# Optimization experiments

Measured on AMD Instinct MI355X. Metric: run time of the kernel, lower is better.

The kernel has to match this reference:

```python
import jax, jax.numpy as jnp
import numpy as np

B, S, D = 4, 2048, 1024
EPS = 1e-5


def setup_inputs() -> dict:
    key = jax.random.key(0)
    ks = jax.random.split(key, 8)
    s = 1.0 / np.sqrt(D)
    return {
        "x": jax.random.normal(ks[0], (B, S, D), dtype=jnp.float32),
        "Wq": jax.random.normal(ks[1], (D, D), dtype=jnp.float32) * s,
        "Wk": jax.random.normal(ks[2], (D, D), dtype=jnp.float32) * s,
        "Wv": jax.random.normal(ks[3], (D, D), dtype=jnp.float32) * s,
        "W1": jax.random.normal(ks[4], (D, D), dtype=jnp.float32) * s,
        "b1": jnp.zeros((D,), dtype=jnp.float32),
        "W2": jax.random.normal(ks[5], (D, D), dtype=jnp.float32) * s,
        "b2": jnp.zeros((D,), dtype=jnp.float32),
        "gamma": jnp.ones((D,), dtype=jnp.float32),
        "beta": jnp.zeros((D,), dtype=jnp.float32),
    }


def _layer_norm(x, gamma, beta):
    mu = jnp.mean(x, axis=-1, keepdims=True)
    var = jnp.mean(jnp.square(x - mu), axis=-1, keepdims=True)
    return (x - mu) * jax.lax.rsqrt(var + EPS) * gamma + beta


def reference(x, Wq, Wk, Wv, W1, b1, W2, b2, gamma, beta):
    seq_len, d = x.shape[1], x.shape[2]
    # torch Linear: y = x @ W.T
    Q = jnp.einsum('bsd,ed->bse', x, Wq)
    K = jnp.einsum('bsd,ed->bse', x, Wk)
    V = jnp.einsum('bsd,ed,->bse', x, Wv, jnp.float32(1.0)) if False else jnp.einsum('bsd,ed->bse', x, Wv)
    scores = jnp.einsum('bqd,bkd->bqk', Q, K) / jnp.sqrt(jnp.float32(d))
    causal = jnp.tril(jnp.ones((seq_len, seq_len), dtype=bool))  # [S,S]
    scores = jnp.where(causal[None, :, :], scores, -jnp.inf)
    attn = jax.nn.softmax(scores, axis=-1)
    attn_out = jnp.einsum('bqk,bkd->bqd', attn, V)
    # dropout is identity at eval
    h = _layer_norm(x + attn_out, gamma, beta)
    ff = jnp.einsum('bsd,ed->bse', jax.nn.relu(jnp.einsum('bsd,ed->bse', h, W1) + b1), W2) + b2
    out = _layer_norm(h + ff, gamma, beta)
    return out
```

## Files before the change

### kernel.cpp

```cpp
#include <hip/hip_runtime.h>
#include <math.h>
#include <cstdint>
#include <cstddef>

#define DI __device__ __forceinline__

typedef __bf16 bf16x8 __attribute__((ext_vector_type(8)));
typedef float f32x4 __attribute__((ext_vector_type(4)));

static constexpr int kB = 4, kS = 2048, kD = 1024;
static constexpr int kM = kB * kS;
static constexpr float kScale = 0.03125f;
static constexpr float kEps = 1e-5f;

DI unsigned short f2bf(float f) {
  unsigned u = __float_as_uint(f);
  u += 0x7FFFu + ((u >> 16) & 1u);
  return (unsigned short)(u >> 16);
}

DI void gld_lds16(const void* g, void* l) {
  __builtin_amdgcn_global_load_lds(
      (__attribute__((address_space(1))) void*)(void*)g,
      (__attribute__((address_space(3))) void*)l, 16, 0, 0);
}

__global__ __launch_bounds__(256) void k_cast_all(
    const float* __restrict__ x, const float* __restrict__ Wq,
    const float* __restrict__ Wk, const float* __restrict__ Wv,
    const float* __restrict__ W1, const float* __restrict__ W2,
    unsigned short* __restrict__ xb, unsigned short* __restrict__ Wqkvb,
    unsigned short* __restrict__ W1b, unsigned short* __restrict__ W2b) {
  const int i = blockIdx.x * 256 + threadIdx.x;
  const int X4 = kM * kD / 4;
  const int W4 = kD * kD / 4;
  const float* src;
  unsigned short* dst;
  int j;
  if (i < X4) { src = x; dst = xb; j = i; }
  else if (i < X4 + W4)     { src = Wq; dst = Wqkvb;           j = i - X4; }
  else if (i < X4 + 2 * W4) { src = Wk; dst = Wqkvb + 4 * W4;  j = i - X4 - W4; }
  else if (i < X4 + 3 * W4) { src = Wv; dst = Wqkvb + 8 * W4;  j = i - X4 - 2 * W4; }
  else if (i < X4 + 4 * W4) { src = W1; dst = W1b;             j = i - X4 - 3 * W4; }
  else                      { src = W2; dst = W2b;             j = i - X4 - 4 * W4; }
  float4 v = ((const float4*)src)[j];
  ushort4 o;
  o.x = f2bf(v.x); o.y = f2bf(v.y); o.z = f2bf(v.z); o.w = f2bf(v.w);
  ((ushort4*)dst)[j] = o;
}

template <int OUT_BF16, int RELU, int CAUSAL>
__global__ __launch_bounds__(256, 2) void k_gemm_nt(
    const unsigned short* __restrict__ A, const unsigned short* __restrict__ B,
    void* __restrict__ Cv, const float* __restrict__ bias,
    int M, int N, int K, int lda, int ldb, int ldc,
    long sA, long sB, long sC) {
  int bm, bn;
  if (CAUSAL == 1) {
    const int t = blockIdx.x;
    int r = (int)floorf((sqrtf(8.f * (float)t + 1.f) - 1.f) * 0.5f);
    while ((r + 1) * (r + 2) / 2 <= t) ++r;
    while (r * (r + 1) / 2 > t) --r;
    bm = r * 128;
    bn = (t - r * (r + 1) / 2) * 128;
  } else if (CAUSAL == 2) {
    bm = (gridDim.y - 1 - blockIdx.y) * 128;
    bn = blockIdx.x * 128;
  } else {
    bm = blockIdx.y * 128;
    bn = blockIdx.x * 128;
  }
  A += (long)blockIdx.z * sA;
  B += (long)blockIdx.z * sB;
  const int Keff = (CAUSAL == 2) ? ((K < bm + 128) ? K : bm + 128) : K;

  const int tid = threadIdx.x;
  const int lane = tid & 63;
  const int wm = ((tid >> 6) >> 1) * 64;
  const int wn = ((tid >> 6) & 1) * 64;

  __shared__ __align__(16) unsigned short Asm[128 * 64];
  __shared__ __align__(16) unsigned short Bsm[128 * 64];

  f32x4 acc[4][4];
#pragma unroll
  for (int i = 0; i < 4; ++i)
#pragma unroll
    for (int j = 0; j < 4; ++j) acc[i][j] = (f32x4){0.f, 0.f, 0.f, 0.f};

  const int r_row = tid >> 3;
  const int dst_k = (tid & 7) * 8;
  const int src_k = ((tid & 7) ^ ((tid >> 3) & 7)) * 8;
  const int fm = lane & 15;
  const int fq = lane >> 4;

  for (int k0 = 0; k0 < Keff; k0 += 64) {
#pragma unroll
    for (int i = 0; i < 4; ++i) {
      const int row = i * 32 + r_row;
      gld_lds16(A + (long)(bm + row) * lda + (k0 + src_k), Asm + row * 64 + dst_k);
      gld_lds16(B + (long)(bn + row) * ldb + (k0 + src_k), Bsm + row * 64 + dst_k);
    }
    __syncthreads();
#pragma unroll
    for (int kk = 0; kk < 2; ++kk) {
      bf16x8 af[4], bfr[4];
#pragma unroll
      for (int i = 0; i < 4; ++i) {
        const int pa = ((kk * 4 + fq) ^ (fm & 7)) * 8;
        af[i]  = *(const bf16x8*)(Asm + (wm + i * 16 + fm) * 64 + pa);
        bfr[i] = *(const bf16x8*)(Bsm + (wn + i * 16 + fm) * 64 + pa);
      }
#pragma unroll
      for (int i = 0; i < 4; ++i)
#pragma unroll
        for (int j = 0; j < 4; ++j)
          acc[i][j] = __builtin_amdgcn_mfma_f32_16x16x32_bf16(af[i], bfr[j], acc[i][j], 0, 0, 0);
    }
    __syncthreads();
  }

  const long cb = (long)blockIdx.z * sC;
#pragma unroll
  for (int i = 0; i < 4; ++i) {
#pragma unroll
    for (int j = 0; j < 4; ++j) {
      const int col = bn + wn + j * 16 + fm;
      const float bv = bias ? bias[col] : 0.f;
#pragma unroll
      for (int r = 0; r < 4; ++r) {
        const int row = bm + wm + i * 16 + fq * 4 + r;
        float v = acc[i][j][r] + bv;
        if (RELU) v = fmaxf(v, 0.f);
        if (OUT_BF16)
          ((unsigned short*)Cv)[cb + (long)row * ldc + col] = f2bf(v);
        else
          ((float*)Cv)[cb + (long)row * ldc + col] = v;
      }
    }
  }
}

DI float wsum(float v) {
  v += __shfl_xor(v, 32, 64);
  v += __shfl_xor(v, 16, 64);
  v += __shfl_xor(v, 8, 64);
  v += __shfl_xor(v, 4, 64);
  v += __shfl_xor(v, 2, 64);
  v += __shfl_xor(v, 1, 64);
  return v;
}
DI float wmax(float v) {
  v = fmaxf(v, __shfl_xor(v, 32, 64));
  v = fmaxf(v, __shfl_xor(v, 16, 64));
  v = fmaxf(v, __shfl_xor(v, 8, 64));
  v = fmaxf(v, __shfl_xor(v, 4, 64));
  v = fmaxf(v, __shfl_xor(v, 2, 64));
  v = fmaxf(v, __shfl_xor(v, 1, 64));
  return v;
}

__global__ __launch_bounds__(256) void k_softmax_causal(const float* __restrict__ S,
                                                        unsigned short* __restrict__ P) {
  const int row = blockIdx.x;
  const int q = row & (kS - 1);
  const int lim = (q & ~127) + 128;
  const float* Srow = S + (long)row * kS;
  unsigned short* Prow = P + (long)row * kS;
  const int tid = threadIdx.x;
  __shared__ float red[4];

  float v[8];
  float mx = -INFINITY;
#pragma unroll
  for (int i = 0; i < 8; ++i) {
    const int k = tid + i * 256;
    float xv = -INFINITY;
    if (k <= q) xv = Srow[k] * kScale;
    v[i] = xv;
    mx = fmaxf(mx, xv);
  }
  mx = wmax(mx);
  if ((tid & 63) == 0) red[tid >> 6] = mx;
  __syncthreads();
  mx = fmaxf(fmaxf(red[0], red[1]), fmaxf(red[2], red[3]));
  __syncthreads();

  float sum = 0.f;
#pragma unroll
  for (int i = 0; i < 8; ++i) {
    const float e = (v[i] > -INFINITY) ? __expf(v[i] - mx) : 0.f;
    v[i] = e;
    sum += e;
  }
  sum = wsum(sum);
  if ((tid & 63) == 0) red[tid >> 6] = sum;
  __syncthreads();
  sum = red[0] + red[1] + red[2] + red[3];
  const float inv = 1.f / sum;
#pragma unroll
  for (int i = 0; i < 8; ++i) {
    const int k = tid + i * 256;
    if (k < lim) Prow[k] = f2bf(v[i] * inv);
  }
}

template <int WRITE_BF16>
__global__ __launch_bounds__(256) void k_residual_ln(
    const float* __restrict__ X, const float* __restrict__ Y,
    const float* __restrict__ gamma, const float* __restrict__ beta,
    float* __restrict__ Out, unsigned short* __restrict__ OutB) {
  const long base = (long)blockIdx.x * kD;
  const int tid = threadIdx.x;
  __shared__ float reds[4], redss[4];
  float v[4];
  float s = 0.f, ss2 = 0.f;
#pragma unroll
  for (int i = 0; i < 4; ++i) {
    const int k = tid + i * 256;
    const float xv = X[base + k] + Y[base + k];
    v[i] = xv;
    s += xv;
    ss2 += xv * xv;
  }
  s = wsum(s);
  ss2 = wsum(ss2);
  if ((tid & 63) == 0) { reds[tid >> 6] = s; redss[tid >> 6] = ss2; }
  __syncthreads();
  s = reds[0] + reds[1] + reds[2] + reds[3];
  ss2 = redss[0] + redss[1] + redss[2] + redss[3];
  const float mu = s * (1.f / kD);
  float var = ss2 * (1.f / kD) - mu * mu;
  var = fmaxf(var, 0.f);
  const float rstd = rsqrtf(var + kEps);
#pragma unroll
  for (int i = 0; i < 4; ++i) {
    const int k = tid + i * 256;
    const float y = (v[i] - mu) * rstd * gamma[k] + beta[k];
    Out[base + k] = y;
    if (WRITE_BF16) OutB[base + k] = f2bf(y);
  }
}

__global__ __launch_bounds__(256) void k_transpose_bf16(
    const unsigned short* __restrict__ in, unsigned short* __restrict__ out,
    int rows, int cols, int ld_in, int ld_out, long sIn, long sOut) {
  __shared__ unsigned short tile[64][65];
  const long ib = (long)blockIdx.z * sIn;
  const long ob = (long)blockIdx.z * sOut;
  const int c0 = blockIdx.x * 64, r0 = blockIdx.y * 64;
  const int tx = threadIdx.x & 63;
  const int ty = threadIdx.x >> 6;
#pragma unroll
  for (int i = 0; i < 16; ++i) {
    const int r = ty + i * 4;
    tile[r][tx] = in[ib + (long)(r0 + r) * ld_in + (c0 + tx)];
  }
  __syncthreads();
#pragma unroll
  for (int i = 0; i < 16; ++i) {
    const int c = ty + i * 4;
    out[ob + (long)(c0 + c) * ld_out + (r0 + tx)] = tile[tx][c];
  }
}

extern "C" void kernel_launch(void* const* d_in, const int* in_sizes, int n_in,
                              void* d_out, int out_size, void* d_ws, size_t ws_size,
                              hipStream_t stream) {
  (void)in_sizes; (void)n_in; (void)out_size; (void)ws_size;
  const float* x     = (const float*)d_in[0];
  const float* Wq    = (const float*)d_in[1];
  const float* Wk    = (const float*)d_in[2];
  const float* Wv    = (const float*)d_in[3];
  const float* W1    = (const float*)d_in[4];
  const float* b1    = (const float*)d_in[5];
  const float* W2    = (const float*)d_in[6];
  const float* b2    = (const float*)d_in[7];
  const float* gamma = (const float*)d_in[8];
  const float* beta  = (const float*)d_in[9];
  float* out = (float*)d_out;

  char* base = (char*)d_ws;
  size_t off = 0;
  auto alloc = [&](size_t bytes) -> void* {
    void* p = base + off;
    off = (off + bytes + 255) & ~(size_t)255;
    return p;
  };

  unsigned short* xb    = (unsigned short*)alloc((size_t)kM * kD * 2);
  unsigned short* Wqkvb = (unsigned short*)alloc((size_t)3 * kD * kD * 2);
  unsigned short* W1b   = (unsigned short*)alloc((size_t)kD * kD * 2);
  unsigned short* W2b   = (unsigned short*)alloc((size_t)kD * kD * 2);
  unsigned short* QKVb  = (unsigned short*)alloc((size_t)kM * 3 * kD * 2);
  unsigned short* Vt    = (unsigned short*)alloc((size_t)kM * kD * 2);
  float*          scores = (float*)alloc((size_t)kB * kS * kS * 4);
  unsigned short* Pb     = (unsigned short*)alloc((size_t)kB * kS * kS * 2);
  float*          h      = (float*)alloc((size_t)kM * kD * 4);
  float* attn = scores;
  float* ff   = (float*)((char*)scores + (size_t)kM * kD * 4);
  unsigned short* hb  = Pb;
  unsigned short* mid = Vt;

  dim3 blk(256);

  {
    const int n4 = (kM * kD + 5 * kD * kD) / 4;
    k_cast_all<<<n4 / 256, blk, 0, stream>>>(x, Wq, Wk, Wv, W1, W2,
                                             xb, Wqkvb, W1b, W2b);
  }

  k_gemm_nt<1, 0, 0><<<dim3(3 * kD / 128, kM / 128, 1), blk, 0, stream>>>(
      xb, Wqkvb, QKVb, nullptr, kM, 3 * kD, kD, kD, kD, 3 * kD, 0, 0, 0);

  k_transpose_bf16<<<dim3(kD / 64, kS / 64, kB), blk, 0, stream>>>(
      QKVb + 2 * kD, Vt, kS, kD, 3 * kD, kS,
      (long)kS * 3 * kD, (long)kD * kS);

  k_gemm_nt<0, 0, 1><<<dim3(136, 1, kB), blk, 0, stream>>>(
      QKVb, QKVb + kD, scores, nullptr, kS, kS, kD, 3 * kD, 3 * kD, kS,
      (long)kS * 3 * kD, (long)kS * 3 * kD, (long)kS * kS);

  k_softmax_causal<<<kM, blk, 0, stream>>>(scores, Pb);

  k_gemm_nt<0, 0, 2><<<dim3(kD / 128, kS / 128, kB), blk, 0, stream>>>(
      Pb, Vt, attn, nullptr, kS, kD, kS, kS, kS, kD,
      (long)kS * kS, (long)kD * kS, (long)kS * kD);

  k_residual_ln<1><<<kM, blk, 0, stream>>>(x, attn, gamma, beta, h, hb);

  k_gemm_nt<1, 1, 0><<<dim3(kD / 128, kM / 128, 1), blk, 0, stream>>>(
      hb, W1b, mid, b1, kM, kD, kD, kD, kD, kD, 0, 0, 0);
  k_gemm_nt<0, 0, 0><<<dim3(kD / 128, kM / 128, 1), blk, 0, stream>>>(
      mid, W2b, ff, b2, kM, kD, kD, kD, kD, kD, 0, 0, 0);

  k_residual_ln<0><<<kM, blk, 0, stream>>>(h, ff, gamma, beta, out, nullptr);
}
```

Measured before the change: 365.3 us.

## Use 32x32 MFMA tiles, compute V transposed directly, store scores in bf16

Switches the GEMM inner loop from 16x16x32 to 32x32x16 bf16 MFMA with 2x2 accumulators per wave, which reduces LDS fragment loads per MFMA. V^T is now produced by a separate GEMM (Wv times x^T per batch), so the standalone transpose kernel is removed. Attention scores are written as bf16 instead of fp32, halving their write and softmax read traffic. The cost is a small loss of precision in the scores before softmax.

After: 363.0 us. About the same (-0.7%).

```diff
diff --git a/kernel.cpp b/kernel.cpp
--- a/kernel.cpp
+++ b/kernel.cpp
@@ -6,7 +6,7 @@
 #define DI __device__ __forceinline__
 
 typedef __bf16 bf16x8 __attribute__((ext_vector_type(8)));
-typedef float f32x4 __attribute__((ext_vector_type(4)));
+typedef float f32x16 __attribute__((ext_vector_type(16)));
 
 static constexpr int kB = 4, kS = 2048, kD = 1024;
 static constexpr int kM = kB * kS;
@@ -18,6 +18,9 @@
   u += 0x7FFFu + ((u >> 16) & 1u);
   return (unsigned short)(u >> 16);
 }
+DI float bf2f(unsigned short h) {
+  return __uint_as_float(((unsigned)h) << 16);
+}
 
 DI void gld_lds16(const void* g, void* l) {
   __builtin_amdgcn_global_load_lds(
@@ -29,8 +32,9 @@
     const float* __restrict__ x, const float* __restrict__ Wq,
     const float* __restrict__ Wk, const float* __restrict__ Wv,
     const float* __restrict__ W1, const float* __restrict__ W2,
-    unsigned short* __restrict__ xb, unsigned short* __restrict__ Wqkvb,
-    unsigned short* __restrict__ W1b, unsigned short* __restrict__ W2b) {
+    unsigned short* __restrict__ xb, unsigned short* __restrict__ Wqkb,
+    unsigned short* __restrict__ Wvb, unsigned short* __restrict__ W1b,
+    unsigned short* __restrict__ W2b) {
   const int i = blockIdx.x * 256 + threadIdx.x;
   const int X4 = kM * kD / 4;
   const int W4 = kD * kD / 4;
@@ -38,11 +42,11 @@
   unsigned short* dst;
   int j;
   if (i < X4) { src = x; dst = xb; j = i; }
-  else if (i < X4 + W4)     { src = Wq; dst = Wqkvb;           j = i - X4; }
-  else if (i < X4 + 2 * W4) { src = Wk; dst = Wqkvb + 4 * W4;  j = i - X4 - W4; }
-  else if (i < X4 + 3 * W4) { src = Wv; dst = Wqkvb + 8 * W4;  j = i - X4 - 2 * W4; }
-  else if (i < X4 + 4 * W4) { src = W1; dst = W1b;             j = i - X4 - 3 * W4; }
-  else                      { src = W2; dst = W2b;             j = i - X4 - 4 * W4; }
+  else if (i < X4 + W4)     { src = Wq; dst = Wqkb;          j = i - X4; }
+  else if (i < X4 + 2 * W4) { src = Wk; dst = Wqkb + 4 * W4; j = i - X4 - W4; }
+  else if (i < X4 + 3 * W4) { src = Wv; dst = Wvb;           j = i - X4 - 2 * W4; }
+  else if (i < X4 + 4 * W4) { src = W1; dst = W1b;           j = i - X4 - 3 * W4; }
+  else                      { src = W2; dst = W2b;           j = i - X4 - 4 * W4; }
   float4 v = ((const float4*)src)[j];
   ushort4 o;
   o.x = f2bf(v.x); o.y = f2bf(v.y); o.z = f2bf(v.z); o.w = f2bf(v.w);
@@ -82,17 +86,19 @@
   __shared__ __align__(16) unsigned short Asm[128 * 64];
   __shared__ __align__(16) unsigned short Bsm[128 * 64];
 
-  f32x4 acc[4][4];
-#pragma unroll
-  for (int i = 0; i < 4; ++i)
-#pragma unroll
-    for (int j = 0; j < 4; ++j) acc[i][j] = (f32x4){0.f, 0.f, 0.f, 0.f};
+  f32x16 acc[2][2];
+#pragma unroll
+  for (int i = 0; i < 2; ++i)
+#pragma unroll
+    for (int j = 0; j < 2; ++j)
+#pragma unroll
+      for (int r = 0; r < 16; ++r) acc[i][j][r] = 0.f;
 
   const int r_row = tid >> 3;
   const int dst_k = (tid & 7) * 8;
   const int src_k = ((tid & 7) ^ ((tid >> 3) & 7)) * 8;
-  const int fm = lane & 15;
-  const int fq = lane >> 4;
+  const int fr = lane & 31;
+  const int fh = lane >> 5;
 
   for (int k0 = 0; k0 < Keff; k0 += 64) {
 #pragma unroll
@@ -103,33 +109,36 @@
     }
     __syncthreads();
 #pragma unroll
-    for (int kk = 0; kk < 2; ++kk) {
-      bf16x8 af[4], bfr[4];
-#pragma unroll
-      for (int i = 0; i < 4; ++i) {
-        const int pa = ((kk * 4 + fq) ^ (fm & 7)) * 8;
-        af[i]  = *(const bf16x8*)(Asm + (wm + i * 16 + fm) * 64 + pa);
-        bfr[i] = *(const bf16x8*)(Bsm + (wn + i * 16 + fm) * 64 + pa);
+    for (int s = 0; s < 4; ++s) {
+      bf16x8 af[2], bfr[2];
+#pragma unroll
+      for (int i = 0; i < 2; ++i) {
+        const int ra = wm + i * 32 + fr;
+        const int rb = wn + i * 32 + fr;
+        const int sa = ((2 * s + fh) ^ (ra & 7)) * 8;
+        const int sb = ((2 * s + fh) ^ (rb & 7)) * 8;
+        af[i]  = *(const bf16x8*)(Asm + ra * 64 + sa);
+        bfr[i] = *(const bf16x8*)(Bsm + rb * 64 + sb);
       }
 #pragma unroll
-      for (int i = 0; i < 4; ++i)
-#pragma unroll
-        for (int j = 0; j < 4; ++j)
-          acc[i][j] = __builtin_amdgcn_mfma_f32_16x16x32_bf16(af[i], bfr[j], acc[i][j], 0, 0, 0);
+      for (int i = 0; i < 2; ++i)
+#pragma unroll
+        for (int j = 0; j < 2; ++j)
+          acc[i][j] = __builtin_amdgcn_mfma_f32_32x32x16_bf16(af[i], bfr[j], acc[i][j], 0, 0, 0);
     }
     __syncthreads();
   }
 
   const long cb = (long)blockIdx.z * sC;
 #pragma unroll
-  for (int i = 0; i < 4; ++i) {
-#pragma unroll
-    for (int j = 0; j < 4; ++j) {
-      const int col = bn + wn + j * 16 + fm;
+  for (int i = 0; i < 2; ++i) {
+#pragma unroll
+    for (int j = 0; j < 2; ++j) {
+      const int col = bn + wn + j * 32 + fr;
       const float bv = bias ? bias[col] : 0.f;
 #pragma unroll
-      for (int r = 0; r < 4; ++r) {
-        const int row = bm + wm + i * 16 + fq * 4 + r;
+      for (int r = 0; r < 16; ++r) {
+        const int row = bm + wm + i * 32 + (r & 3) + 8 * (r >> 2) + 4 * fh;
         float v = acc[i][j][r] + bv;
         if (RELU) v = fmaxf(v, 0.f);
         if (OUT_BF16)
@@ -160,12 +169,12 @@
   return v;
 }
 
-__global__ __launch_bounds__(256) void k_softmax_causal(const float* __restrict__ S,
-                                                        unsigned short* __restrict__ P) {
+__global__ __launch_bounds__(256) void k_softmax_causal(
+    const unsigned short* __restrict__ S, unsigned short* __restrict__ P) {
   const int row = blockIdx.x;
   const int q = row & (kS - 1);
   const int lim = (q & ~127) + 128;
-  const float* Srow = S + (long)row * kS;
+  const unsigned short* Srow = S + (long)row * kS;
   unsigned short* Prow = P + (long)row * kS;
   const int tid = threadIdx.x;
   __shared__ float red[4];
@@ -176,7 +185,7 @@
   for (int i = 0; i < 8; ++i) {
     const int k = tid + i * 256;
     float xv = -INFINITY;
-    if (k <= q) xv = Srow[k] * kScale;
+    if (k <= q) xv = bf2f(Srow[k]) * kScale;
     v[i] = xv;
     mx = fmaxf(mx, xv);
   }
@@ -239,28 +248,6 @@
     const float y = (v[i] - mu) * rstd * gamma[k] + beta[k];
     Out[base + k] = y;
     if (WRITE_BF16) OutB[base + k] = f2bf(y);
-  }
-}
-
-__global__ __launch_bounds__(256) void k_transpose_bf16(
-    const unsigned short* __restrict__ in, unsigned short* __restrict__ out,
-    int rows, int cols, int ld_in, int ld_out, long sIn, long sOut) {
-  __shared__ unsigned short tile[64][65];
-  const long ib = (long)blockIdx.z * sIn;
-  const long ob = (long)blockIdx.z * sOut;
-  const int c0 = blockIdx.x * 64, r0 = blockIdx.y * 64;
-  const int tx = threadIdx.x & 63;
-  const int ty = threadIdx.x >> 6;
-#pragma unroll
-  for (int i = 0; i < 16; ++i) {
-    const int r = ty + i * 4;
-    tile[r][tx] = in[ib + (long)(r0 + r) * ld_in + (c0 + tx)];
-  }
-  __syncthreads();
-#pragma unroll
-  for (int i = 0; i < 16; ++i) {
-    const int c = ty + i * 4;
-    out[ob + (long)(c0 + c) * ld_out + (r0 + tx)] = tile[tx][c];
   }
 }
 
@@ -288,40 +275,41 @@
     return p;
   };
 
-  unsigned short* xb    = (unsigned short*)alloc((size_t)kM * kD * 2);
-  unsigned short* Wqkvb = (unsigned short*)alloc((size_t)3 * kD * kD * 2);
-  unsigned short* W1b   = (unsigned short*)alloc((size_t)kD * kD * 2);
-  unsigned short* W2b   = (unsigned short*)alloc((size_t)kD * kD * 2);
-  unsigned short* QKVb  = (unsigned short*)alloc((size_t)kM * 3 * kD * 2);
-  unsigned short* Vt    = (unsigned short*)alloc((size_t)kM * kD * 2);
-  float*          scores = (float*)alloc((size_t)kB * kS * kS * 4);
-  unsigned short* Pb     = (unsigned short*)alloc((size_t)kB * kS * kS * 2);
-  float*          h      = (float*)alloc((size_t)kM * kD * 4);
-  float* attn = scores;
-  float* ff   = (float*)((char*)scores + (size_t)kM * kD * 4);
-  unsigned short* hb  = Pb;
-  unsigned short* mid = Vt;
+  unsigned short* xb   = (unsigned short*)alloc((size_t)kM * kD * 2);
+  unsigned short* Wqkb = (unsigned short*)alloc((size_t)2 * kD * kD * 2);
+  unsigned short* Wvb  = (unsigned short*)alloc((size_t)kD * kD * 2);
+  unsigned short* W1b  = (unsigned short*)alloc((size_t)kD * kD * 2);
+  unsigned short* W2b  = (unsigned short*)alloc((size_t)kD * kD * 2);
+  unsigned short* QKb  = (unsigned short*)alloc((size_t)kM * 2 * kD * 2);
+  unsigned short* Vt   = (unsigned short*)alloc((size_t)kM * kD * 2);
+  unsigned short* Sb   = (unsigned short*)alloc((size_t)kB * kS * kS * 2);
+  unsigned short* Pb   = (unsigned short*)alloc((size_t)kB * kS * kS * 2);
+  float*          attn = (float*)alloc((size_t)kM * kD * 4);
+  float*          h    = (float*)alloc((size_t)kM * kD * 4);
+  float*          ff   = attn;
+  unsigned short* hb   = Sb;
+  unsigned short* mid  = Pb;
 
   dim3 blk(256);
 
   {
     const int n4 = (kM * kD + 5 * kD * kD) / 4;
     k_cast_all<<<n4 / 256, blk, 0, stream>>>(x, Wq, Wk, Wv, W1, W2,
-                                             xb, Wqkvb, W1b, W2b);
-  }
-
-  k_gemm_nt<1, 0, 0><<<dim3(3 * kD / 128, kM / 128, 1), blk, 0, stream>>>(
-      xb, Wqkvb, QKVb, nullptr, kM, 3 * kD, kD, kD, kD, 3 * kD, 0, 0, 0);
-
-  k_transpose_bf16<<<dim3(kD / 64, kS / 64, kB), blk, 0, stream>>>(
-      QKVb + 2 * kD, Vt, kS, kD, 3 * kD, kS,
-      (long)kS * 3 * kD, (long)kD * kS);
-
-  k_gemm_nt<0, 0, 1><<<dim3(136, 1, kB), blk, 0, stream>>>(
-      QKVb, QKVb + kD, scores, nullptr, kS, kS, kD, 3 * kD, 3 * kD, kS,
-      (long)kS * 3 * kD, (long)kS * 3 * kD, (long)kS * kS);
-
-  k_softmax_causal<<<kM, blk, 0, stream>>>(scores, Pb);
+                                             xb, Wqkb, Wvb, W1b, W2b);
+  }
+
+  k_gemm_nt<1, 0, 0><<<dim3(2 * kD / 128, kM / 128, 1), blk, 0, stream>>>(
+      xb, Wqkb, QKb, nullptr, kM, 2 * kD, kD, kD, kD, 2 * kD, 0, 0, 0);
+
+  k_gemm_nt<1, 0, 0><<<dim3(kS / 128, kD / 128, kB), blk, 0, stream>>>(
+      Wvb, xb, Vt, nullptr, kD, kS, kD, kD, kD, kS,
+      0, (long)kS * kD, (long)kD * kS);
+
+  k_gemm_nt<1, 0, 1><<<dim3(136, 1, kB), blk, 0, stream>>>(
+      QKb, QKb + kD, Sb, nullptr, kS, kS, kD, 2 * kD, 2 * kD, kS,
+      (long)kS * 2 * kD, (long)kS * 2 * kD, (long)kS * kS);
+
+  k_softmax_causal<<<kM, blk, 0, stream>>>(Sb, Pb);
 
   k_gemm_nt<0, 0, 2><<<dim3(kD / 128, kS / 128, kB), blk, 0, stream>>>(
       Pb, Vt, attn, nullptr, kS, kD, kS, kS, kS, kD,
```
